# Optimization experiments

Hardware: AMD Instinct MI355X
Metric: run time of the kernel (lower is better)

The kernel has to match this reference:

```python
import jax, jax.numpy as jnp
import numpy as np

B, T, D_MODEL = 4, 1024, 1024
H, DQK, DV = 16, 64, 64
POS_NUM = 2 * T - 1  # 2047
SCALE = 0.05  # keep softmax logits in a sane range for random weights


def setup_inputs() -> dict:
    key = jax.random.key(0)
    ks = jax.random.split(key, 8)
    x = jax.random.normal(ks[0], (B, T, D_MODEL), dtype=jnp.float32)
    W_Q = jax.random.normal(ks[1], (H, DQK, DQK), dtype=jnp.float32) * SCALE
    W_K = jax.random.normal(ks[2], (H, DQK, DQK), dtype=jnp.float32) * SCALE
    W_V = jax.random.normal(ks[3], (H, DQK, DV), dtype=jnp.float32) * SCALE
    W_Z = jax.random.normal(ks[4], (H * DV, D_MODEL), dtype=jnp.float32) * SCALE
    pos_K_emb = jax.random.normal(ks[5], (POS_NUM, DQK), dtype=jnp.float32) * SCALE
    pos_V_emb = jax.random.normal(ks[6], (POS_NUM, DV), dtype=jnp.float32) * SCALE
    mask = jnp.zeros((T, T), dtype=jnp.float32)  # additive attention mask
    pos = jax.random.randint(ks[7], (T, T), 0, POS_NUM, dtype=jnp.int32)
    return {"x": x, "W_Q": W_Q, "W_K": W_K, "W_V": W_V, "W_Z": W_Z,
            "pos_K_emb": pos_K_emb, "pos_V_emb": pos_V_emb,
            "mask": mask, "pos": pos}


def reference(x, W_Q, W_K, W_V, W_Z, pos_K_emb, pos_V_emb, mask, pos):
    Bs, Ts, _ = x.shape
    h, dqk, dv = W_V.shape
    # [B,T,D] -> [B,H,T,dQK]
    xh = x.reshape(Bs, Ts, h, dqk).transpose(0, 2, 1, 3)
    Q = jnp.einsum('bhtd,hde->bhte', xh, W_Q)
    K = jnp.einsum('bhtd,hde->bhte', xh, W_K)
    V = jnp.einsum('bhtd,hde->bhte', xh, W_V)
    # content scores + relative-position key bias
    PK = pos_K_emb[pos]                       # [T,T,dQK]
    scores = jnp.einsum('bhqd,bhkd->bhqk', Q, K)
    scores = scores + jnp.einsum('bhqd,qkd->bhqk', Q, PK)
    # NOTE: original adds mask BEFORE dividing by sqrt(dQK); replicate exactly
    scores = (scores + mask) / jnp.sqrt(jnp.asarray(dqk, dtype=scores.dtype))
    attn = jax.nn.softmax(scores, axis=-1)    # [B,H,T,T]
    ctx = jnp.einsum('bhqk,bhkd->bhqd', attn, V)
    PV = pos_V_emb[pos]                       # [T,T,dV]
    ctx = ctx + jnp.einsum('bhqk,qkd->bhqd', attn, PV)
    out = ctx.transpose(0, 2, 1, 3).reshape(Bs, Ts, h * dv)
    return out @ W_Z
```

## Files before the change

### kernel.cpp

```cpp
#include <hip/hip_runtime.h>
#include <hip/hip_bf16.h>

#define BB 4
#define TT 1024
#define DM 1024
#define HH 16

typedef __attribute__((ext_vector_type(8))) short short8;
typedef __attribute__((ext_vector_type(4))) short short4v;
typedef __attribute__((ext_vector_type(4))) float f32x4;
typedef __hip_bfloat16 bf16;
typedef unsigned char u8;

__device__ __forceinline__ f32x4 mfma16(short8 a, short8 b, f32x4 c) {
  return __builtin_amdgcn_mfma_f32_16x16x32_bf16(a, b, c, 0, 0, 0);
}
__device__ __forceinline__ f32x4 mfma8(long a, long b, f32x4 c) {
  return __builtin_amdgcn_mfma_f32_16x16x32_fp8_fp8(a, b, c, 0, 0, 0);
}

__global__ __launch_bounds__(256) void pack_pm_kernel(
    const int* __restrict__ pos, const float* __restrict__ maskp,
    unsigned* __restrict__ pm) {
  const size_t i = (size_t)blockIdx.x * 256 + threadIdx.x;
  const unsigned mb = __float_as_uint(maskp[i]) & 0xffff0000u;
  pm[i] = mb | (unsigned)pos[i];
}

__global__ __launch_bounds__(256) void prep_w_kernel(
    const float* __restrict__ WQ, const float* __restrict__ WK,
    const float* __restrict__ WV, bf16* __restrict__ Wt) {
  __shared__ bf16 tl[64][72];
  const int h = blockIdx.x, m = blockIdx.y;
  const float* W = (m == 0 ? WQ : (m == 1 ? WK : WV)) + h * 4096;
  const int tid = threadIdx.x;
  const int r = tid >> 2, c = (tid & 3) * 16;
#pragma unroll
  for (int i = 0; i < 16; ++i)
    tl[r][c + i] = __float2bfloat16(W[r * 64 + c + i]);
  __syncthreads();
  bf16* o = Wt + ((size_t)(m * 16 + h) * 64 + r) * 64 + c;
#pragma unroll
  for (int i = 0; i < 16; ++i) o[i] = tl[c + i][r];
}

__global__ __launch_bounds__(256) void prep_posk8_kernel(
    const float* __restrict__ posK, u8* __restrict__ posK8) {
  const int idx = (blockIdx.x * 256 + threadIdx.x) * 2;
  const int p = idx >> 6, d = idx & 63;
  const float v0 = (p < 2047) ? posK[(size_t)p * 64 + d] : 0.f;
  const float v1 = (p < 2047) ? posK[(size_t)p * 64 + d + 1] : 0.f;
  const int pk = __builtin_amdgcn_cvt_pk_fp8_f32(v0, v1, 0, false);
  *(unsigned short*)(posK8 + idx) = (unsigned short)(pk & 0xffff);
}

__global__ __launch_bounds__(256) void trans_wz_kernel(
    const float* __restrict__ Wz, bf16* __restrict__ WzT) {
  __shared__ bf16 tile[64][72];
  const int k0 = blockIdx.y * 64, n0 = blockIdx.x * 64;
  const int tid = threadIdx.x;
  const int r = tid >> 2, c = (tid & 3) * 16;
  const float* s = Wz + (size_t)(k0 + r) * 1024 + n0 + c;
#pragma unroll
  for (int i = 0; i < 16; ++i) tile[r][c + i] = __float2bfloat16(s[i]);
  __syncthreads();
  const int n = tid >> 2;
  bf16* o = WzT + (size_t)(n0 + n) * 1024 + k0 + c;
#pragma unroll
  for (int i = 0; i < 16; ++i) o[i] = tile[c + i][n];
}

__global__ __launch_bounds__(256) void trans_v_kernel(
    const bf16* __restrict__ src, bf16* __restrict__ dst) {
  __shared__ bf16 tile[64][72];
  const int bh = blockIdx.y, t0 = blockIdx.x * 64;
  const int tid = threadIdx.x;
  const int r = tid >> 2, c = (tid & 3) * 16;
  const bf16* s = src + ((size_t)bh * TT + t0 + r) * 64 + c;
  *(short8*)(&tile[r][c]) = *(const short8*)(s);
  *(short8*)(&tile[r][c + 8]) = *(const short8*)(s + 8);
  __syncthreads();
  const int d = tid >> 2;
  bf16* o = dst + ((size_t)bh * 64 + d) * TT + t0 + c;
#pragma unroll
  for (int i = 0; i < 16; ++i) o[i] = tile[c + i][d];
}

__global__ __launch_bounds__(256) void qkv_mfma_kernel(
    const float* __restrict__ x, const bf16* __restrict__ Wt,
    u8* __restrict__ Q8, u8* __restrict__ K8, bf16* __restrict__ Vg) {
  __shared__ __align__(16) bf16 xs[64 * 72];
  const int bh = blockIdx.y;
  const int b = bh >> 4, h = bh & 15;
  const int t0 = blockIdx.x * 64;
  const int tid = threadIdx.x;
  const int w = tid >> 6, lane = tid & 63, l15 = lane & 15, hi = lane >> 4;

  {
    const int r = tid >> 2, c = (tid & 3) * 16;
    const float* src = x + ((size_t)b * TT + t0 + r) * DM + h * 64 + c;
    bf16 tmp[16];
#pragma unroll
    for (int i = 0; i < 16; i += 4) {
      const f32x4 v = *(const f32x4*)(src + i);
      tmp[i + 0] = __float2bfloat16(v[0]);
      tmp[i + 1] = __float2bfloat16(v[1]);
      tmp[i + 2] = __float2bfloat16(v[2]);
      tmp[i + 3] = __float2bfloat16(v[3]);
    }
    *(short8*)(xs + r * 72 + c) = *(const short8*)tmp;
    *(short8*)(xs + r * 72 + c + 8) = *(const short8*)(tmp + 8);
  }
  __syncthreads();

  f32x4 aQ[4] = {{0.f, 0.f, 0.f, 0.f}, {0.f, 0.f, 0.f, 0.f},
                 {0.f, 0.f, 0.f, 0.f}, {0.f, 0.f, 0.f, 0.f}};
  f32x4 aK[4] = {{0.f, 0.f, 0.f, 0.f}, {0.f, 0.f, 0.f, 0.f},
                 {0.f, 0.f, 0.f, 0.f}, {0.f, 0.f, 0.f, 0.f}};
  f32x4 aV[4] = {{0.f, 0.f, 0.f, 0.f}, {0.f, 0.f, 0.f, 0.f},
                 {0.f, 0.f, 0.f, 0.f}, {0.f, 0.f, 0.f, 0.f}};
  const bf16* WtQ = Wt + (size_t)h * 4096;
  const bf16* WtK = Wt + (size_t)(16 + h) * 4096;
  const bf16* WtV = Wt + (size_t)(32 + h) * 4096;
#pragma unroll
  for (int kc = 0; kc < 2; ++kc) {
    const short8 a =
        *(const short8*)(xs + (w * 16 + l15) * 72 + kc * 32 + hi * 8);
#pragma unroll
    for (int nt = 0; nt < 4; ++nt) {
      const size_t wo = (size_t)(nt * 16 + l15) * 64 + kc * 32 + hi * 8;
      aQ[nt] = mfma16(a, *(const short8*)(WtQ + wo), aQ[nt]);
      aK[nt] = mfma16(a, *(const short8*)(WtK + wo), aK[nt]);
      aV[nt] = mfma16(a, *(const short8*)(WtV + wo), aV[nt]);
    }
  }
  const int t = t0 + w * 16 + hi * 4;
#pragma unroll
  for (int nt = 0; nt < 4; ++nt) {
#pragma unroll
    for (int j = 0; j < 4; ++j) {
      const size_t o = ((size_t)bh * TT + t + j) * 64 + nt * 16 + l15;
      Vg[o] = __float2bfloat16(aV[nt][j]);
    }
    const size_t o0 = ((size_t)bh * TT + t) * 64 + nt * 16 + l15;
    {
      const int p01 = __builtin_amdgcn_cvt_pk_fp8_f32(aQ[nt][0], aQ[nt][1], 0, false);
      const int p23 = __builtin_amdgcn_cvt_pk_fp8_f32(aQ[nt][2], aQ[nt][3], 0, false);
      Q8[o0] = (u8)(p01 & 0xff);
      Q8[o0 + 64] = (u8)((p01 >> 8) & 0xff);
      Q8[o0 + 128] = (u8)(p23 & 0xff);
      Q8[o0 + 192] = (u8)((p23 >> 8) & 0xff);
    }
    {
      const int p01 = __builtin_amdgcn_cvt_pk_fp8_f32(aK[nt][0], aK[nt][1], 0, false);
      const int p23 = __builtin_amdgcn_cvt_pk_fp8_f32(aK[nt][2], aK[nt][3], 0, false);
      K8[o0] = (u8)(p01 & 0xff);
      K8[o0 + 64] = (u8)((p01 >> 8) & 0xff);
      K8[o0 + 128] = (u8)(p23 & 0xff);
      K8[o0 + 192] = (u8)((p23 >> 8) & 0xff);
    }
  }
}

#define QP8_S 2052
#define PSM_S 72

__global__ __launch_bounds__(256, 1) void score_pv_kernel(
    const u8* __restrict__ Q8,
    const u8* __restrict__ K8,
    const u8* __restrict__ posK8,
    const bf16* __restrict__ Vt,
    const unsigned* __restrict__ pm,
    bf16* __restrict__ Pws,
    float* __restrict__ l_ws,
    float* __restrict__ ctxU,
    int slab) {
  __shared__ __align__(16) u8 QPsh[64 * QP8_S];
  __shared__ __align__(16) bf16 Psm[2][64 * PSM_S];
  __shared__ float lred[4][64];

  const int bh = blockIdx.x;
  const int qt = blockIdx.y;
  const int qlocal0 = qt * 64;
  const int qg0 = slab * 256 + qlocal0;
  const int tid = threadIdx.x;
  const int w = tid >> 6;
  const int lane = tid & 63;
  const int l15 = lane & 15;
  const int hi = lane >> 4;

  long aqA[4], aqB[4];
#pragma unroll
  for (int h = 0; h < 4; ++h) {
    const u8* Qrow = Q8 + ((size_t)bh * TT + qg0 + h * 16 + l15) * 64;
    aqA[h] = *(const long*)(Qrow + hi * 8);
    aqB[h] = *(const long*)(Qrow + 32 + hi * 8);
  }

  {
    const u8* Kp0 = posK8 + (size_t)(w * 32 * 16 + l15) * 64;
    long qb0 = *(const long*)(Kp0 + hi * 8);
    long qb1 = *(const long*)(Kp0 + 32 + hi * 8);
    for (int i = 0; i < 32; ++i) {
      const int pt = w * 32 + i;
      const long cb0 = qb0, cb1 = qb1;
      {
        const int ptn = w * 32 + ((i + 1) & 31);
        const u8* Kpn = posK8 + (size_t)(ptn * 16 + l15) * 64;
        qb0 = *(const long*)(Kpn + hi * 8);
        qb1 = *(const long*)(Kpn + 32 + hi * 8);
      }
      const int off = pt * 16 + l15;
#pragma unroll
      for (int h = 0; h < 4; ++h) {
        f32x4 a4 = {0.f, 0.f, 0.f, 0.f};
        a4 = mfma8(aqA[h], cb0, a4);
        a4 = mfma8(aqB[h], cb1, a4);
        const int p01 = __builtin_amdgcn_cvt_pk_fp8_f32(a4[0], a4[1], 0, false);
        const int p23 = __builtin_amdgcn_cvt_pk_fp8_f32(a4[2], a4[3], 0, false);
        const int qr = h * 16 + hi * 4;
        QPsh[(qr + 0) * QP8_S + off] = (u8)(p01 & 0xff);
        QPsh[(qr + 1) * QP8_S + off] = (u8)((p01 >> 8) & 0xff);
        QPsh[(qr + 2) * QP8_S + off] = (u8)(p23 & 0xff);
        QPsh[(qr + 3) * QP8_S + off] = (u8)((p23 >> 8) & 0xff);
      }
    }
  }
  __syncthreads();

  f32x4 acc[4] = {{0.f, 0.f, 0.f, 0.f}, {0.f, 0.f, 0.f, 0.f},
                  {0.f, 0.f, 0.f, 0.f}, {0.f, 0.f, 0.f, 0.f}};
  float lp[16];
#pragma unroll
  for (int j = 0; j < 16; ++j) lp[j] = 0.f;
  const int kk = w * 16 + l15;
  const u8* K8bh = K8 + (size_t)bh * TT * 64;
  const bf16* Vtrow = Vt + ((size_t)bh * 64 + w * 16 + l15) * TT;

  long nb0 = *(const long*)(K8bh + (size_t)kk * 64 + hi * 8);
  long nb1 = *(const long*)(K8bh + (size_t)kk * 64 + 32 + hi * 8);
  short8 nv0 = *(const short8*)(Vtrow + hi * 8);
  short8 nv1 = *(const short8*)(Vtrow + 32 + hi * 8);
  unsigned npm[16];
#pragma unroll
  for (int h = 0; h < 4; ++h)
#pragma unroll
    for (int j = 0; j < 4; ++j)
      npm[h * 4 + j] = pm[(size_t)(qg0 + h * 16 + hi * 4 + j) * TT + kk];

  for (int it = 0; it < 16; ++it) {
    const int k0 = it * 64;
    bf16* PsmC = &Psm[it & 1][0];
    const long cb0 = nb0, cb1 = nb1;
    const short8 cv0 = nv0, cv1 = nv1;
    unsigned cpm[16];
#pragma unroll
    for (int j = 0; j < 16; ++j) cpm[j] = npm[j];
    {
      const int k0n = ((it + 1) & 15) * 64;
      nb0 = *(const long*)(K8bh + (size_t)(k0n + kk) * 64 + hi * 8);
      nb1 = *(const long*)(K8bh + (size_t)(k0n + kk) * 64 + 32 + hi * 8);
      nv0 = *(const short8*)(Vtrow + k0n + hi * 8);
      nv1 = *(const short8*)(Vtrow + k0n + 32 + hi * 8);
#pragma unroll
      for (int h = 0; h < 4; ++h)
#pragma unroll
        for (int j = 0; j < 4; ++j)
          npm[h * 4 + j] =
              pm[(size_t)(qg0 + h * 16 + hi * 4 + j) * TT + k0n + kk];
    }
#pragma unroll
    for (int h = 0; h < 4; ++h) {
      f32x4 s = {0.f, 0.f, 0.f, 0.f};
      s = mfma8(aqA[h], cb0, s);
      s = mfma8(aqB[h], cb1, s);
#pragma unroll
      for (int j = 0; j < 4; ++j) {
        const int q = h * 16 + hi * 4 + j;
        const unsigned pmv = cpm[h * 4 + j];
        const float qp = __builtin_amdgcn_cvt_f32_fp8(
            (int)QPsh[q * QP8_S + (pmv & 0xffffu)], 0);
        const float sv =
            (s[j] + qp + __uint_as_float(pmv & 0xffff0000u)) * 0.125f;
        const float pe = __expf(sv);
        lp[h * 4 + j] += pe;
        PsmC[q * PSM_S + kk] = __float2bfloat16(pe);
      }
    }
    __syncthreads();
    {
      const int r = tid >> 2, c = (tid & 3) * 16;
      *(short8*)(Pws + ((size_t)(qlocal0 + r) * 64 + bh) * TT + k0 + c) =
          *(const short8*)(PsmC + r * PSM_S + c);
      *(short8*)(Pws + ((size_t)(qlocal0 + r) * 64 + bh) * TT + k0 + c + 8) =
          *(const short8*)(PsmC + r * PSM_S + c + 8);
    }
#pragma unroll
    for (int h = 0; h < 4; ++h) {
      const short8 pa0 =
          *(const short8*)(PsmC + (h * 16 + l15) * PSM_S + hi * 8);
      acc[h] = mfma16(pa0, cv0, acc[h]);
      const short8 pa1 =
          *(const short8*)(PsmC + (h * 16 + l15) * PSM_S + 32 + hi * 8);
      acc[h] = mfma16(pa1, cv1, acc[h]);
    }
  }

#pragma unroll
  for (int j = 0; j < 16; ++j) {
    float v = lp[j];
    v += __shfl_xor(v, 1);
    v += __shfl_xor(v, 2);
    v += __shfl_xor(v, 4);
    v += __shfl_xor(v, 8);
    lp[j] = v;
  }
  __syncthreads();
  if (l15 == 0) {
#pragma unroll
    for (int h = 0; h < 4; ++h)
#pragma unroll
      for (int j = 0; j < 4; ++j) lred[w][h * 16 + hi * 4 + j] = lp[h * 4 + j];
  }
  __syncthreads();
  if (tid < 64) {
    const float l = lred[0][tid] + lred[1][tid] + lred[2][tid] + lred[3][tid];
    l_ws[(size_t)bh * TT + qg0 + tid] = l;
  }
  {
    const int b = bh >> 4, h16 = bh & 15;
#pragma unroll
    for (int h = 0; h < 4; ++h)
#pragma unroll
      for (int j = 0; j < 4; ++j) {
        const int q = h * 16 + hi * 4 + j;
        ctxU[((size_t)b * TT + qg0 + q) * DM + h16 * 64 + w * 16 + l15] =
            acc[h][j];
      }
  }
}

#define PVT_S 72
__global__ __launch_bounds__(256) void pv_part_kernel(
    const bf16* __restrict__ Pws,
    const float* __restrict__ posV,
    const unsigned* __restrict__ pm,
    float* __restrict__ PP,
    int slab) {
  __shared__ __align__(16) bf16 PVt[2][64 * PVT_S];
  __shared__ unsigned short possh[512];

  const int qlocal = blockIdx.x;
  const int q = slab * 256 + qlocal;
  const int ks = blockIdx.y;
  const int kbase = ks * 512;
  const int tid = threadIdx.x;
  const int w = tid >> 6, lane = tid & 63, l15 = lane & 15, hi = lane >> 4;

  possh[tid] = (unsigned short)(pm[(size_t)q * TT + kbase + tid] & 0xffffu);
  possh[256 + tid] =
      (unsigned short)(pm[(size_t)q * TT + kbase + 256 + tid] & 0xffffu);
  __syncthreads();

  f32x4 acc[4] = {{0.f, 0.f, 0.f, 0.f}, {0.f, 0.f, 0.f, 0.f},
                  {0.f, 0.f, 0.f, 0.f}, {0.f, 0.f, 0.f, 0.f}};
  const bf16* Prow = Pws + ((size_t)qlocal * 64 + w * 16 + l15) * TT;

  for (int it = 0; it < 8; ++it) {
    const int k0 = kbase + it * 64;
    bf16* pvt = &PVt[it & 1][0];
    {
      const int kr = lane;
      const int dc = w * 16;
      const int p = possh[it * 64 + kr];
      const float* src = posV + (size_t)p * 64 + dc;
#pragma unroll
      for (int ii = 0; ii < 16; ii += 4) {
        const f32x4 v = *(const f32x4*)(src + ii);
        pvt[(dc + ii + 0) * PVT_S + kr] = __float2bfloat16(v[0]);
        pvt[(dc + ii + 1) * PVT_S + kr] = __float2bfloat16(v[1]);
        pvt[(dc + ii + 2) * PVT_S + kr] = __float2bfloat16(v[2]);
        pvt[(dc + ii + 3) * PVT_S + kr] = __float2bfloat16(v[3]);
      }
    }
    __syncthreads();
#pragma unroll
    for (int kc = 0; kc < 2; ++kc) {
      const short8 a = *(const short8*)(Prow + k0 + kc * 32 + hi * 8);
#pragma unroll
      for (int nt = 0; nt < 4; ++nt) {
        const short8 bv =
            *(const short8*)(pvt + (nt * 16 + l15) * PVT_S + kc * 32 + hi * 8);
        acc[nt] = mfma16(a, bv, acc[nt]);
      }
    }
  }

  const int bh0 = w * 16 + hi * 4;
#pragma unroll
  for (int j = 0; j < 4; ++j) {
    const int bh = bh0 + j;
    float* o = PP + (((size_t)ks * 256 + qlocal) * 64 + bh) * 64;
#pragma unroll
    for (int nt = 0; nt < 4; ++nt) o[nt * 16 + l15] = acc[nt][j];
  }
}

__global__ __launch_bounds__(256) void norm_kernel(
    const float* __restrict__ PP,
    const float* __restrict__ ctxU,
    const float* __restrict__ l_ws,
    bf16* __restrict__ ctxB,
    int slab) {
  const int i4 = blockIdx.x * 256 + threadIdx.x;
  const int e0 = i4 * 4;
  const int dm = e0 & 1023;
  const int qlocal = (e0 >> 10) & 255;
  const int b = e0 >> 18;
  const int h = dm >> 6, d0 = dm & 63;
  const int bh = b * 16 + h;
  const int q = slab * 256 + qlocal;

  f32x4 v = *(const f32x4*)(ctxU + ((size_t)b * TT + q) * DM + dm);
#pragma unroll
  for (int ks = 0; ks < 2; ++ks)
    v += *(const f32x4*)(PP + (((size_t)ks * 256 + qlocal) * 64 + bh) * 64 + d0);
  const float invl = 1.0f / l_ws[(size_t)bh * TT + q];
  bf16 o[4];
#pragma unroll
  for (int j = 0; j < 4; ++j) o[j] = __float2bfloat16(v[j] * invl);
  *(short4v*)(ctxB + ((size_t)b * TT + q) * DM + dm) = *(const short4v*)o;
}

__global__ __launch_bounds__(256) void outproj_mfma_kernel(
    const bf16* __restrict__ A,
    const bf16* __restrict__ Bt,
    float* __restrict__ C) {
  __shared__ __align__(16) bf16 As[128 * 72];
  __shared__ __align__(16) bf16 Bs[128 * 72];
  const int n0 = blockIdx.x * 128;
  const int m0 = blockIdx.y * 128;
  const int tid = threadIdx.x;
  const int w = tid >> 6, lane = tid & 63, l15 = lane & 15, hi = lane >> 4;
  const int wm = w >> 1, wn = w & 1;

  f32x4 acc[4][4];
#pragma unroll
  for (int i = 0; i < 4; ++i)
#pragma unroll
    for (int j = 0; j < 4; ++j) acc[i][j] = (f32x4){0.f, 0.f, 0.f, 0.f};

  const int sr = tid >> 1, sc = (tid & 1) * 32;
  for (int k0 = 0; k0 < 1024; k0 += 64) {
    __syncthreads();
    {
      const bf16* as = A + (size_t)(m0 + sr) * 1024 + k0 + sc;
      const bf16* bs = Bt + (size_t)(n0 + sr) * 1024 + k0 + sc;
#pragma unroll
      for (int ii = 0; ii < 32; ii += 8) {
        *(short8*)(As + sr * 72 + sc + ii) = *(const short8*)(as + ii);
        *(short8*)(Bs + sr * 72 + sc + ii) = *(const short8*)(bs + ii);
      }
    }
    __syncthreads();
#pragma unroll
    for (int kc = 0; kc < 2; ++kc) {
      short8 a[4], b[4];
#pragma unroll
      for (int i = 0; i < 4; ++i)
        a[i] = *(const short8*)(As + (wm * 64 + i * 16 + l15) * 72 + kc * 32 +
                                hi * 8);
#pragma unroll
      for (int j = 0; j < 4; ++j)
        b[j] = *(const short8*)(Bs + (wn * 64 + j * 16 + l15) * 72 + kc * 32 +
                                hi * 8);
#pragma unroll
      for (int i = 0; i < 4; ++i)
#pragma unroll
        for (int j = 0; j < 4; ++j) acc[i][j] = mfma16(a[i], b[j], acc[i][j]);
    }
  }
#pragma unroll
  for (int i = 0; i < 4; ++i) {
#pragma unroll
    for (int jj = 0; jj < 4; ++jj) {
      const size_t row = (size_t)(m0 + wm * 64 + i * 16 + hi * 4 + jj) * 1024;
#pragma unroll
      for (int j = 0; j < 4; ++j)
        C[row + n0 + wn * 64 + j * 16 + l15] = acc[i][j][jj];
    }
  }
}

extern "C" void kernel_launch(void* const* d_in, const int* in_sizes, int n_in,
                              void* d_out, int out_size, void* d_ws,
                              size_t ws_size, hipStream_t stream) {
  const float* x = (const float*)d_in[0];
  const float* WQ = (const float*)d_in[1];
  const float* WK = (const float*)d_in[2];
  const float* WV = (const float*)d_in[3];
  const float* WZ = (const float*)d_in[4];
  const float* posK = (const float*)d_in[5];
  const float* posV = (const float*)d_in[6];
  const float* maskp = (const float*)d_in[7];
  const int* pos = (const int*)d_in[8];
  float* out = (float*)d_out;

  char* p = (char*)d_ws;
  u8* Q8 = (u8*)p;            p += (size_t)64 * 1024 * 64;
  u8* K8 = (u8*)p;            p += (size_t)64 * 1024 * 64;
  bf16* Vb = (bf16*)p;        p += (size_t)64 * 1024 * 64 * 2;
  bf16* Vt = (bf16*)p;        p += (size_t)64 * 64 * 1024 * 2;
  u8* posK8 = (u8*)p;         p += (size_t)2048 * 64;
  bf16* WzT = (bf16*)p;       p += (size_t)1024 * 1024 * 2;
  bf16* Pws = (bf16*)p;       p += (size_t)256 * 64 * 1024 * 2;
  float* l_ws = (float*)p;    p += (size_t)64 * 1024 * 4;
  float* ctxU = (float*)p;    p += (size_t)4 * 1024 * 1024 * 4;
  bf16* ctxB = (bf16*)p;      p += (size_t)4 * 1024 * 1024 * 2;
  float* PP = (float*)p;      p += (size_t)2 * 256 * 64 * 64 * 4;
  unsigned* pm_ws = (unsigned*)p; p += (size_t)1024 * 1024 * 4;

  bf16* Wt = ctxB;

  pack_pm_kernel<<<4096, 256, 0, stream>>>(pos, maskp, pm_ws);
  prep_w_kernel<<<dim3(16, 3), 256, 0, stream>>>(WQ, WK, WV, Wt);
  prep_posk8_kernel<<<256, 256, 0, stream>>>(posK, posK8);
  trans_wz_kernel<<<dim3(16, 16), 256, 0, stream>>>(WZ, WzT);
  qkv_mfma_kernel<<<dim3(16, 64), 256, 0, stream>>>(x, Wt, Q8, K8, Vb);
  trans_v_kernel<<<dim3(16, 64), 256, 0, stream>>>(Vb, Vt);

  for (int slab = 0; slab < 4; ++slab) {
    score_pv_kernel<<<dim3(64, 4), 256, 0, stream>>>(
        Q8, K8, posK8, Vt, pm_ws, Pws, l_ws, ctxU, slab);
    pv_part_kernel<<<dim3(256, 2), 256, 0, stream>>>(Pws, posV, pm_ws, PP,
                                                     slab);
    norm_kernel<<<1024, 256, 0, stream>>>(PP, ctxU, l_ws, ctxB, slab);
  }
  outproj_mfma_kernel<<<dim3(8, 32), 256, 0, stream>>>(ctxB, WzT, out);
}
```

Before: 272.5 us.

## Fuse V transpose into QKV, merge PV-part with normalization, use exp2

The QKV projection kernel now transposes V through shared memory and writes Vt directly, which removes the separate transpose kernel and the intermediate V buffer. The positional-V partial kernel now covers all 1024 keys in one block and applies the ctxU add and the 1/l normalization itself, so the PP workspace and the norm kernel are gone. The softmax exponent uses exp2f with a folded log2(e)/8 scale. The trade-offs are half as many PV blocks per slab, with a longer serial loop that now has an added barrier per iteration, and uncoalesced scalar writes to ctxB.

```diff
diff --git a/kernel.cpp b/kernel.cpp
--- a/kernel.cpp
+++ b/kernel.cpp
@@ -18,6 +18,8 @@
 __device__ __forceinline__ f32x4 mfma8(long a, long b, f32x4 c) {
   return __builtin_amdgcn_mfma_f32_16x16x32_fp8_fp8(a, b, c, 0, 0, 0);
 }
+
+#define EXP2SCALE 0.1803368801111244f
 
 __global__ __launch_bounds__(256) void pack_pm_kernel(
     const int* __restrict__ pos, const float* __restrict__ maskp,
@@ -70,25 +72,9 @@
   for (int i = 0; i < 16; ++i) o[i] = tile[c + i][n];
 }
 
-__global__ __launch_bounds__(256) void trans_v_kernel(
-    const bf16* __restrict__ src, bf16* __restrict__ dst) {
-  __shared__ bf16 tile[64][72];
-  const int bh = blockIdx.y, t0 = blockIdx.x * 64;
-  const int tid = threadIdx.x;
-  const int r = tid >> 2, c = (tid & 3) * 16;
-  const bf16* s = src + ((size_t)bh * TT + t0 + r) * 64 + c;
-  *(short8*)(&tile[r][c]) = *(const short8*)(s);
-  *(short8*)(&tile[r][c + 8]) = *(const short8*)(s + 8);
-  __syncthreads();
-  const int d = tid >> 2;
-  bf16* o = dst + ((size_t)bh * 64 + d) * TT + t0 + c;
-#pragma unroll
-  for (int i = 0; i < 16; ++i) o[i] = tile[c + i][d];
-}
-
 __global__ __launch_bounds__(256) void qkv_mfma_kernel(
     const float* __restrict__ x, const bf16* __restrict__ Wt,
-    u8* __restrict__ Q8, u8* __restrict__ K8, bf16* __restrict__ Vg) {
+    u8* __restrict__ Q8, u8* __restrict__ K8, bf16* __restrict__ Vt) {
   __shared__ __align__(16) bf16 xs[64 * 72];
   const int bh = blockIdx.y;
   const int b = bh >> 4, h = bh & 15;
@@ -137,11 +123,6 @@
   const int t = t0 + w * 16 + hi * 4;
 #pragma unroll
   for (int nt = 0; nt < 4; ++nt) {
-#pragma unroll
-    for (int j = 0; j < 4; ++j) {
-      const size_t o = ((size_t)bh * TT + t + j) * 64 + nt * 16 + l15;
-      Vg[o] = __float2bfloat16(aV[nt][j]);
-    }
     const size_t o0 = ((size_t)bh * TT + t) * 64 + nt * 16 + l15;
     {
       const int p01 = __builtin_amdgcn_cvt_pk_fp8_f32(aQ[nt][0], aQ[nt][1], 0, false);
@@ -159,6 +140,20 @@
       K8[o0 + 128] = (u8)(p23 & 0xff);
       K8[o0 + 192] = (u8)((p23 >> 8) & 0xff);
     }
+  }
+  __syncthreads();
+#pragma unroll
+  for (int nt = 0; nt < 4; ++nt)
+#pragma unroll
+    for (int j = 0; j < 4; ++j)
+      xs[(nt * 16 + l15) * 72 + w * 16 + hi * 4 + j] =
+          __float2bfloat16(aV[nt][j]);
+  __syncthreads();
+  {
+    const int r = tid >> 2, c = (tid & 3) * 16;
+    bf16* o = Vt + ((size_t)bh * 64 + r) * TT + t0 + c;
+    *(short8*)(o) = *(const short8*)(xs + r * 72 + c);
+    *(short8*)(o + 8) = *(const short8*)(xs + r * 72 + c + 8);
   }
 }
 
@@ -281,8 +276,8 @@
         const float qp = __builtin_amdgcn_cvt_f32_fp8(
             (int)QPsh[q * QP8_S + (pmv & 0xffffu)], 0);
         const float sv =
-            (s[j] + qp + __uint_as_float(pmv & 0xffff0000u)) * 0.125f;
-        const float pe = __expf(sv);
+            (s[j] + qp + __uint_as_float(pmv & 0xffff0000u)) * EXP2SCALE;
+        const float pe = exp2f(sv);
         lp[h * 4 + j] += pe;
         PsmC[q * PSM_S + kk] = __float2bfloat16(pe);
       }
@@ -341,38 +336,39 @@
 }
 
 #define PVT_S 72
-__global__ __launch_bounds__(256) void pv_part_kernel(
+__global__ __launch_bounds__(256) void pv_fused_kernel(
     const bf16* __restrict__ Pws,
     const float* __restrict__ posV,
     const unsigned* __restrict__ pm,
-    float* __restrict__ PP,
+    const float* __restrict__ l_ws,
+    const float* __restrict__ ctxU,
+    bf16* __restrict__ ctxB,
     int slab) {
   __shared__ __align__(16) bf16 PVt[2][64 * PVT_S];
-  __shared__ unsigned short possh[512];
+  __shared__ unsigned short possh[1024];
 
   const int qlocal = blockIdx.x;
   const int q = slab * 256 + qlocal;
-  const int ks = blockIdx.y;
-  const int kbase = ks * 512;
   const int tid = threadIdx.x;
   const int w = tid >> 6, lane = tid & 63, l15 = lane & 15, hi = lane >> 4;
 
-  possh[tid] = (unsigned short)(pm[(size_t)q * TT + kbase + tid] & 0xffffu);
-  possh[256 + tid] =
-      (unsigned short)(pm[(size_t)q * TT + kbase + 256 + tid] & 0xffffu);
+#pragma unroll
+  for (int i = 0; i < 4; ++i)
+    possh[i * 256 + tid] =
+        (unsigned short)(pm[(size_t)q * TT + i * 256 + tid] & 0xffffu);
   __syncthreads();
 
   f32x4 acc[4] = {{0.f, 0.f, 0.f, 0.f}, {0.f, 0.f, 0.f, 0.f},
                   {0.f, 0.f, 0.f, 0.f}, {0.f, 0.f, 0.f, 0.f}};
   const bf16* Prow = Pws + ((size_t)qlocal * 64 + w * 16 + l15) * TT;
 
-  for (int it = 0; it < 8; ++it) {
-    const int k0 = kbase + it * 64;
+  for (int it = 0; it < 16; ++it) {
+    const int k0 = it * 64;
     bf16* pvt = &PVt[it & 1][0];
     {
       const int kr = lane;
       const int dc = w * 16;
-      const int p = possh[it * 64 + kr];
+      const int p = possh[k0 + kr];
       const float* src = posV + (size_t)p * 64 + dc;
 #pragma unroll
       for (int ii = 0; ii < 16; ii += 4) {
@@ -394,42 +390,22 @@
         acc[nt] = mfma16(a, bv, acc[nt]);
       }
     }
+    __syncthreads();
   }
 
   const int bh0 = w * 16 + hi * 4;
 #pragma unroll
   for (int j = 0; j < 4; ++j) {
     const int bh = bh0 + j;
-    float* o = PP + (((size_t)ks * 256 + qlocal) * 64 + bh) * 64;
-#pragma unroll
-    for (int nt = 0; nt < 4; ++nt) o[nt * 16 + l15] = acc[nt][j];
-  }
-}
-
-__global__ __launch_bounds__(256) void norm_kernel(
-    const float* __restrict__ PP,
-    const float* __restrict__ ctxU,
-    const float* __restrict__ l_ws,
-    bf16* __restrict__ ctxB,
-    int slab) {
-  const int i4 = blockIdx.x * 256 + threadIdx.x;
-  const int e0 = i4 * 4;
-  const int dm = e0 & 1023;
-  const int qlocal = (e0 >> 10) & 255;
-  const int b = e0 >> 18;
-  const int h = dm >> 6, d0 = dm & 63;
-  const int bh = b * 16 + h;
-  const int q = slab * 256 + qlocal;
-
-  f32x4 v = *(const f32x4*)(ctxU + ((size_t)b * TT + q) * DM + dm);
-#pragma unroll
-  for (int ks = 0; ks < 2; ++ks)
-    v += *(const f32x4*)(PP + (((size_t)ks * 256 + qlocal) * 64 + bh) * 64 + d0);
-  const float invl = 1.0f / l_ws[(size_t)bh * TT + q];
-  bf16 o[4];
-#pragma unroll
-  for (int j = 0; j < 4; ++j) o[j] = __float2bfloat16(v[j] * invl);
-  *(short4v*)(ctxB + ((size_t)b * TT + q) * DM + dm) = *(const short4v*)o;
+    const int b = bh >> 4, h16 = bh & 15;
+    const float invl = 1.0f / l_ws[(size_t)bh * TT + q];
+    const size_t base = ((size_t)b * TT + q) * DM + h16 * 64;
+#pragma unroll
+    for (int nt = 0; nt < 4; ++nt) {
+      const size_t o = base + nt * 16 + l15;
+      ctxB[o] = __float2bfloat16((ctxU[o] + acc[nt][j]) * invl);
+    }
+  }
 }
 
 __global__ __launch_bounds__(256) void outproj_mfma_kernel(
@@ -509,7 +485,6 @@
   char* p = (char*)d_ws;
   u8* Q8 = (u8*)p;            p += (size_t)64 * 1024 * 64;
   u8* K8 = (u8*)p;            p += (size_t)64 * 1024 * 64;
-  bf16* Vb = (bf16*)p;        p += (size_t)64 * 1024 * 64 * 2;
   bf16* Vt = (bf16*)p;        p += (size_t)64 * 64 * 1024 * 2;
   u8* posK8 = (u8*)p;         p += (size_t)2048 * 64;
   bf16* WzT = (bf16*)p;       p += (size_t)1024 * 1024 * 2;
@@ -517,7 +492,6 @@
   float* l_ws = (float*)p;    p += (size_t)64 * 1024 * 4;
   float* ctxU = (float*)p;    p += (size_t)4 * 1024 * 1024 * 4;
   bf16* ctxB = (bf16*)p;      p += (size_t)4 * 1024 * 1024 * 2;
-  float* PP = (float*)p;      p += (size_t)2 * 256 * 64 * 64 * 4;
   unsigned* pm_ws = (unsigned*)p; p += (size_t)1024 * 1024 * 4;
 
   bf16* Wt = ctxB;
@@ -526,15 +500,13 @@
   prep_w_kernel<<<dim3(16, 3), 256, 0, stream>>>(WQ, WK, WV, Wt);
   prep_posk8_kernel<<<256, 256, 0, stream>>>(posK, posK8);
   trans_wz_kernel<<<dim3(16, 16), 256, 0, stream>>>(WZ, WzT);
-  qkv_mfma_kernel<<<dim3(16, 64), 256, 0, stream>>>(x, Wt, Q8, K8, Vb);
-  trans_v_kernel<<<dim3(16, 64), 256, 0, stream>>>(Vb, Vt);
+  qkv_mfma_kernel<<<dim3(16, 64), 256, 0, stream>>>(x, Wt, Q8, K8, Vt);
 
   for (int slab = 0; slab < 4; ++slab) {
     score_pv_kernel<<<dim3(64, 4), 256, 0, stream>>>(
         Q8, K8, posK8, Vt, pm_ws, Pws, l_ws, ctxU, slab);
-    pv_part_kernel<<<dim3(256, 2), 256, 0, stream>>>(Pws, posV, pm_ws, PP,
-                                                     slab);
-    norm_kernel<<<1024, 256, 0, stream>>>(PP, ctxU, l_ws, ctxB, slab);
+    pv_fused_kernel<<<256, 256, 0, stream>>>(Pws, posV, pm_ws, l_ws, ctxU,
+                                             ctxB, slab);
   }
   outproj_mfma_kernel<<<dim3(8, 32), 256, 0, stream>>>(ctxB, WzT, out);
 }
```

New measurement: 292.8 us. 7.5% more time.
